# Performance work log

Hardware: AMD Instinct MI355X
Metric: run time of the kernel (lower is better)

Reference implementation:

```python
import jax, jax.numpy as jnp
import numpy as np

B, S, D = 4, 2048, 2048


def setup_inputs() -> dict:
    key = jax.random.key(0)
    ks = jax.random.split(key, 24)
    sc = 1.0 / np.sqrt(D)
    def lin(ki, kb):
        W = jax.random.normal(ks[ki], (D, D), dtype=jnp.float32) * sc
        b = jax.random.normal(ks[kb], (D,), dtype=jnp.float32) * 0.01
        return W, b
    Wi, bWi = lin(0, 1); Ui, bUi = lin(2, 3)
    Wf, bWf = lin(4, 5); Uf, bUf = lin(6, 7)
    Wc, bWc = lin(8, 9); Uc, bUc = lin(10, 11)
    Wo, bWo = lin(12, 13); Uo, bUo = lin(14, 15)
    Wp, bp = lin(16, 17)
    x = jax.random.normal(ks[18], (B, S, D), dtype=jnp.float32)
    h = jax.random.normal(ks[19], (B, S, D), dtype=jnp.float32)
    return dict(x=x, h=h, Wi=Wi, bWi=bWi, Ui=Ui, bUi=bUi,
                Wf=Wf, bWf=bWf, Uf=Uf, bUf=bUf,
                Wc=Wc, bWc=bWc, Uc=Uc, bUc=bUc,
                Wo=Wo, bWo=bWo, Uo=Uo, bUo=bUo,
                Wp=Wp, bp=bp)


def reference(x, h, Wi, bWi, Ui, bUi, Wf, bWf, Uf, bUf,
              Wc, bWc, Uc, bUc, Wo, bWo, Uo, bUo, Wp, bp):
    # In the torch source, h[:, t, :] is read BEFORE being overwritten at step t,
    # and c is zero-initialized with each slot written once (so f * c_prev == 0).
    # Hence the computation is exactly parallel over the time axis.
    Zi = jnp.einsum('bsd,ed->bse', x, Wi) + bWi + jnp.einsum('bsd,ed->bse', h, Ui) + bUi
    Zf = jnp.einsum('bsd,ed->bse', x, Wf) + bWf + jnp.einsum('bsd,ed->bse', h, Uf) + bUf
    Zc = jnp.einsum('bsd,ed->bse', x, Wc) + bWc + jnp.einsum('bsd,ed->bse', h, Uc) + bUc
    Zo = jnp.einsum('bsd,ed->bse', x, Wo) + bWo + jnp.einsum('bsd,ed->bse', h, Uo) + bUo
    i = jnp.exp(Zi)
    f = jnp.exp(Zf)  # multiplies a zero cell state in the source; kept for fidelity
    c = f * jnp.zeros_like(f) + i * jnp.tanh(Zc)
    h_out = jax.nn.sigmoid(Zo) * jnp.tanh(c)
    hidden_state = h_out[:, -1, :] @ Wp.T + bp
    return (hidden_state, c)
```

## Files before the change

### kernel.cpp

```cpp
#include <hip/hip_runtime.h>
#include <hip/hip_bf16.h>

typedef short short8 __attribute__((ext_vector_type(8)));
typedef unsigned short ushort8v __attribute__((ext_vector_type(8)));
typedef float f32x4 __attribute__((ext_vector_type(4)));

#define D_DIM 2048
#define KTOT 4096
#define M_TOT 8192
#define NPACK 4096


__device__ __forceinline__ unsigned short f2bf(float f) {
    union { float f; unsigned u; } c; c.f = f;
    unsigned u = c.u;
    u += 0x7fffu + ((u >> 16) & 1u);
    return (unsigned short)(u >> 16);
}

__device__ __forceinline__ float fast_tanh(float x) {
    float ax = fabsf(x);
    float ez = __expf(2.0f * fminf(ax, 15.0f));
    float t = (ez - 1.0f) / (ez + 1.0f);
    return copysignf(t, x);
}

#define GLOAD_LDS16(g, l)                                                     \
    __builtin_amdgcn_global_load_lds(                                         \
        (const __attribute__((address_space(1))) void*)(g),                   \
        (__attribute__((address_space(3))) void*)(l), 16, 0, 0)

#define WAITVM_(N) asm volatile("s_waitcnt vmcnt(" #N ")" ::: "memory")
#define WAITVM(N)  WAITVM_(N)
#define WAITLG_(N) asm volatile("s_waitcnt lgkmcnt(" #N ")" ::: "memory")
#define WAITLG(N)  WAITLG_(N)
#define BAR        __builtin_amdgcn_s_barrier()
#define SCHB       __builtin_amdgcn_sched_barrier(0)
#define PRIO1      __builtin_amdgcn_s_setprio(1)
#define PRIO0      __builtin_amdgcn_s_setprio(0)


__global__ __launch_bounds__(256)
void pack2(const float* __restrict__ X, const float* __restrict__ H,
           __hip_bfloat16* __restrict__ dst, int total8) {
    int t = blockIdx.x * 256 + threadIdx.x;
    if (t >= total8) return;
    long e0 = (long)t * 8;
    long r  = e0 >> 12;
    int  k  = (int)(e0 & 4095);
    const float* src = (k < D_DIM) ? (X + r * D_DIM + k)
                                   : (H + r * D_DIM + (k - D_DIM));
    float4 v0 = *(const float4*)(src);
    float4 v1 = *(const float4*)(src + 4);
    ushort8v o;
    o[0] = f2bf(v0.x); o[1] = f2bf(v0.y); o[2] = f2bf(v0.z); o[3] = f2bf(v0.w);
    o[4] = f2bf(v1.x); o[5] = f2bf(v1.y); o[6] = f2bf(v1.z); o[7] = f2bf(v1.w);
    *(ushort8v*)(dst + e0) = o;
}


__global__ __launch_bounds__(256)
void pack_gates(const float* __restrict__ Wi, const float* __restrict__ Ui,
                const float* __restrict__ Wc, const float* __restrict__ Uc,
                __hip_bfloat16* __restrict__ dst) {
    int t = blockIdx.x * 256 + threadIdx.x;
    const int g = t >> 9;
    const int k = (t & 511) * 8;
    const int w = g & 31;
    const int n = ((g >> 5) << 4) | (w & 15);
    const float* Wm = (w & 16) ? Wc : Wi;
    const float* Um = (w & 16) ? Uc : Ui;
    const float* src = (k < D_DIM) ? (Wm + (size_t)n * D_DIM + k)
                                   : (Um + (size_t)n * D_DIM + (k - D_DIM));
    float4 v0 = *(const float4*)(src);
    float4 v1 = *(const float4*)(src + 4);
    ushort8v o;
    o[0] = f2bf(v0.x); o[1] = f2bf(v0.y); o[2] = f2bf(v0.z); o[3] = f2bf(v0.w);
    o[4] = f2bf(v1.x); o[5] = f2bf(v1.y); o[6] = f2bf(v1.z); o[7] = f2bf(v1.w);
    *(ushort8v*)(dst + (size_t)g * KTOT + k) = o;
}


__device__ __forceinline__ f32x4 mf(short8 a, short8 b, f32x4 c) {
    return __builtin_amdgcn_mfma_f32_16x16x32_bf16(a, b, c, 0, 0, 0);
}

#define RD4A(BUF, IMM)                                                        \
  { _Pragma("unroll") for (int m_ = 0; m_ < 4; ++m_) {                        \
      ak0[m_] = *(const short8*)(rdA0 + (BUF) + (IMM) + m_ * 2048);           \
      ak1[m_] = *(const short8*)(rdA1 + (BUF) + (IMM) + m_ * 2048); } }

#define RDB(d0, d1, BUF, IMM)                                                 \
  { _Pragma("unroll") for (int n_ = 0; n_ < 2; ++n_) {                        \
      d0[n_] = *(const short8*)(rdB0 + (BUF) + (IMM) + n_ * 2048);            \
      d1[n_] = *(const short8*)(rdB1 + (BUF) + (IMM) + n_ * 2048); } }

#define MF16(MB, NB, bk0, bk1)                                                \
  { _Pragma("unroll") for (int m_ = 0; m_ < 4; ++m_)                          \
    _Pragma("unroll") for (int n_ = 0; n_ < 2; ++n_)                          \
      acc[(MB)+m_][(NB)+n_] = mf(ak0[m_], bk0[n_], acc[(MB)+m_][(NB)+n_]);    \
    _Pragma("unroll") for (int m_ = 0; m_ < 4; ++m_)                          \
    _Pragma("unroll") for (int n_ = 0; n_ < 2; ++n_)                          \
      acc[(MB)+m_][(NB)+n_] = mf(ak1[m_], bk1[n_], acc[(MB)+m_][(NB)+n_]); }

#define SA0(BUFB, KB) { GLOAD_LDS16(gAh0 + (KB), ldsA + (BUFB) + dOff);       \
                        GLOAD_LDS16(gAh0 + (KB) + 524288, ldsA + (BUFB) + dOff + 8192); }
#define SA1(BUFB, KB) { GLOAD_LDS16(gAh1 + (KB), ldsA + (BUFB) + 16384 + dOff); \
                        GLOAD_LDS16(gAh1 + (KB) + 524288, ldsA + (BUFB) + 16384 + dOff + 8192); }
#define SB0(BUFB, KB) { GLOAD_LDS16(gBh0 + (KB), ldsB + (BUFB) + dOff);       \
                        GLOAD_LDS16(gBh0 + (KB) + 524288, ldsB + (BUFB) + dOff + 8192); }
#define SB1(BUFB, KB) { GLOAD_LDS16(gBh1 + (KB), ldsB + (BUFB) + 16384 + dOff); \
                        GLOAD_LDS16(gBh1 + (KB) + 524288, ldsB + (BUFB) + 16384 + dOff + 8192); }

#define KTILE(BUF, S1, S2, S3, S4, VMN)                                       \
  {            \
    RD4A(BUF, 0);                                                             \
    RDB(b01k0, b01k1, BUF, 0);                                                \
    S1;                                                                       \
    WAITLG(8);                                                                \
    BAR; WAITLG(0); SCHB;                                                     \
    PRIO1; MF16(0, 0, b01k0, b01k1); PRIO0; BAR;                              \
                                 \
    RDB(b23k0, b23k1, BUF, 4096);                                             \
    S2;                                                                       \
    BAR; WAITLG(0); SCHB;                                                     \
    PRIO1; MF16(0, 2, b23k0, b23k1); PRIO0; BAR;                              \
                                 \
    RD4A(BUF, 8192);                                                          \
    S3;                                                                       \
    BAR; WAITLG(0); SCHB;                                                     \
    PRIO1; MF16(4, 0, b01k0, b01k1); PRIO0; BAR;                              \
                          \
    S4; VMN;                                                                  \
    BAR; SCHB;                                                                \
    PRIO1; MF16(4, 2, b23k0, b23k1); PRIO0; BAR;                              \
  }

#define NOSTG (void)0

__global__ __launch_bounds__(512, 2)
void gemm8(const __hip_bfloat16* __restrict__ A,
           const __hip_bfloat16* __restrict__ Bp,
           const float* __restrict__ bWi, const float* __restrict__ bUi,
           const float* __restrict__ bWc, const float* __restrict__ bUc,
           float* __restrict__ Cout) {
    __shared__ __hip_bfloat16 sA[2][2][128][64];
    __shared__ __hip_bfloat16 sB[2][2][128][64];

    const int tid  = threadIdx.x;
    const int wid  = tid >> 6;
    const int lane = tid & 63;

    int bid = blockIdx.x;
    bid = (bid & 7) * 64 + (bid >> 3);
    const int tn = (bid & 15) * 256;
    const int tm = (bid >> 4) * 256;

    const int wr  = (wid >> 2) * 128;
    const int wc  = (wid & 3) * 64;
    const int r15 = lane & 15;
    const int g   = lane >> 4;

    const int sb    = g ^ (r15 & 3);
    const int khb   = (r15 >> 2) & 1;
    const int slot0 = (khb * 4 + sb) * 16;
    const int slot1 = (((1 ^ khb) * 4) + sb) * 16;

    const char* rdA0 = (const char*)sA + (wr >> 7) * 16384 + r15 * 128 + slot0;
    const char* rdA1 = (const char*)sA + (wr >> 7) * 16384 + r15 * 128 + slot1;
    const char* rdB0 = (const char*)sB + (wc >> 7) * 16384 + (wc & 64) * 128 + r15 * 128 + slot0;
    const char* rdB1 = (const char*)sB + (wc >> 7) * 16384 + (wc & 64) * 128 + r15 * 128 + slot1;

    const int r0 = tid >> 3, s0 = tid & 7;
    const int colb = (((s0 >> 2) ^ ((r0 >> 2) & 1)) * 64) +
                     (((s0 & 3) ^ (r0 & 3)) * 16);
    const char* gAh0 = (const char*)(A  + (size_t)(tm + r0) * KTOT) + colb;
    const char* gAh1 = gAh0 + (size_t)128 * KTOT * 2;
    const char* gBh0 = (const char*)(Bp + (size_t)(tn + r0) * KTOT) + colb;
    const char* gBh1 = gBh0 + (size_t)128 * KTOT * 2;
    char* ldsA = (char*)sA;
    char* ldsB = (char*)sB;
    const int dOff = tid * 16;

    f32x4 acc[8][4] = {};
    short8 ak0[4], ak1[4], b01k0[2], b01k1[2], b23k0[2], b23k1[2];

    SB0(0, 0); SB1(0, 0); SA0(0, 0); SA1(0, 0);
    SB0(32768, 128); SB1(32768, 128);
    WAITVM(4);
    BAR;

    int kb = 0;
    #pragma unroll 1
    for (int i = 0; i < 31; ++i) {
        KTILE(0,
              SA0(32768, kb + 128), SA1(32768, kb + 128),
              SB0(0, kb + 256),     SB1(0, kb + 256),
              WAITVM(4));
        KTILE(32768,
              SA0(0, kb + 256),     SA1(0, kb + 256),
              SB0(32768, kb + 384), SB1(32768, kb + 384),
              WAITVM(4));
        kb += 256;
    }
    KTILE(0, SA0(32768, kb + 128), SA1(32768, kb + 128),
          NOSTG, NOSTG, WAITVM(0));
    KTILE(32768, NOSTG, NOSTG, NOSTG, NOSTG, NOSTG);

    const int rg4 = (lane >> 4) * 4;
    #pragma unroll
    for (int q = 0; q < 2; ++q) {
        const int gn = (tn >> 1) + (wc >> 1) + q * 16 + r15;
        const float bi_ = bWi[gn] + bUi[gn];
        const float bc_ = bWc[gn] + bUc[gn];
        #pragma unroll
        for (int m = 0; m < 8; ++m) {
            const int gm = tm + wr + m * 16 + rg4;
            #pragma unroll
            for (int r = 0; r < 4; ++r) {
                const float zi = acc[m][2 * q][r]     + bi_;
                const float zc = acc[m][2 * q + 1][r] + bc_;
                Cout[(size_t)(gm + r) * D_DIM + gn] = __expf(zi) * fast_tanh(zc);
            }
        }
    }
}


__global__ __launch_bounds__(256)
void last_gate(const float* __restrict__ x, const float* __restrict__ h,
               const float* __restrict__ Wo, const float* __restrict__ bWo,
               const float* __restrict__ Uo, const float* __restrict__ bUo,
               const float* __restrict__ cfull, float* __restrict__ hbuf) {
    const int o    = blockIdx.x * 4 + (threadIdx.x >> 6);
    const int lane = threadIdx.x & 63;
    const int b = o >> 11, e = o & 2047;
    const float* xr = x  + ((size_t)b * D_DIM + (D_DIM - 1)) * D_DIM;
    const float* hr = h  + ((size_t)b * D_DIM + (D_DIM - 1)) * D_DIM;
    const float* wo = Wo + (size_t)e * D_DIM;
    const float* uo = Uo + (size_t)e * D_DIM;
    float s = 0.0f;
    for (int d = lane; d < D_DIM; d += 64)
        s += xr[d] * wo[d] + hr[d] * uo[d];
    #pragma unroll
    for (int off = 32; off; off >>= 1) s += __shfl_down(s, off);
    if (lane == 0) {
        const float zo  = s + bWo[e] + bUo[e];
        const float sig = 1.0f / (1.0f + __expf(-zo));
        const float cv  = cfull[((size_t)b * D_DIM + (D_DIM - 1)) * D_DIM + e];
        hbuf[o] = sig * fast_tanh(cv);
    }
}


__global__ __launch_bounds__(256)
void proj(const float* __restrict__ hbuf, const float* __restrict__ Wp,
          const float* __restrict__ bp, float* __restrict__ out) {
    const int o    = blockIdx.x * 4 + (threadIdx.x >> 6);
    const int lane = threadIdx.x & 63;
    const int b = o >> 11, p = o & 2047;
    const float* hv = hbuf + (size_t)b * D_DIM;
    const float* wp = Wp   + (size_t)p * D_DIM;
    float s = 0.0f;
    for (int e = lane; e < D_DIM; e += 64)
        s += hv[e] * wp[e];
    #pragma unroll
    for (int off = 32; off; off >>= 1) s += __shfl_down(s, off);
    if (lane == 0) out[o] = s + bp[p];
}


extern "C" void kernel_launch(void* const* d_in, const int* in_sizes, int n_in,
                              void* d_out, int out_size, void* d_ws, size_t ws_size,
                              hipStream_t stream) {
    const float* x   = (const float*)d_in[0];
    const float* h   = (const float*)d_in[1];
    const float* Wi  = (const float*)d_in[2];  const float* bWi = (const float*)d_in[3];
    const float* Ui  = (const float*)d_in[4];  const float* bUi = (const float*)d_in[5];
    const float* Wc  = (const float*)d_in[10]; const float* bWc = (const float*)d_in[11];
    const float* Uc  = (const float*)d_in[12]; const float* bUc = (const float*)d_in[13];
    const float* Wo  = (const float*)d_in[14]; const float* bWo = (const float*)d_in[15];
    const float* Uo  = (const float*)d_in[16]; const float* bUo = (const float*)d_in[17];
    const float* Wp  = (const float*)d_in[18]; const float* bp  = (const float*)d_in[19];

    float* out = (float*)d_out;
    char*  ws  = (char*)d_ws;

    __hip_bfloat16* Abf  = (__hip_bfloat16*)ws;
    __hip_bfloat16* Bpk  = (__hip_bfloat16*)(ws + ((size_t)64 << 20));
    float*          hbuf = (float*)(ws + ((size_t)96 << 20));

    pack2<<<16384, 256, 0, stream>>>(x, h, Abf, M_TOT * KTOT / 8);
    pack_gates<<<8192, 256, 0, stream>>>(Wi, Ui, Wc, Uc, Bpk);

    gemm8<<<(M_TOT / 256) * (NPACK / 256), 512, 0, stream>>>(
        Abf, Bpk, bWi, bUi, bWc, bUc, out + 8192);

    last_gate<<<2048, 256, 0, stream>>>(x, h, Wo, bWo, Uo, bUo, out + 8192,
                                        (float*)hbuf);
    proj<<<2048, 256, 0, stream>>>(hbuf, Wp, bp, out);
}
```

Measured before the change: 320.3 us.

## Triple-buffer A tiles in LDS and deepen prefetch pipeline for GEMM

Allocates a third LDS buffer for the A operand, so A is prefetched two k-tiles ahead while B stays double-buffered. The main loop becomes a six-tile rotation and all global-to-LDS loads are moved into the later stages of each k-tile. Launch bounds drop from 2 to 1 blocks per CU to fit the extra LDS. The intent is to hide more global-load latency, at the cost of occupancy and a more complex wait-count schedule.

```diff
diff --git a/kernel.cpp b/kernel.cpp
--- a/kernel.cpp
+++ b/kernel.cpp
@@ -85,15 +85,15 @@
     return __builtin_amdgcn_mfma_f32_16x16x32_bf16(a, b, c, 0, 0, 0);
 }
 
-#define RD4A(BUF, IMM)                                                        \
+#define RD4A(RGO, IMM)                                                        \
   { _Pragma("unroll") for (int m_ = 0; m_ < 4; ++m_) {                        \
-      ak0[m_] = *(const short8*)(rdA0 + (BUF) + (IMM) + m_ * 2048);           \
-      ak1[m_] = *(const short8*)(rdA1 + (BUF) + (IMM) + m_ * 2048); } }
-
-#define RDB(d0, d1, BUF, IMM)                                                 \
+      ak0[m_] = *(const short8*)(rdA0 + (RGO) + (IMM) + m_ * 2048);           \
+      ak1[m_] = *(const short8*)(rdA1 + (RGO) + (IMM) + m_ * 2048); } }
+
+#define RDB(d0, d1, BFO, IMM)                                                 \
   { _Pragma("unroll") for (int n_ = 0; n_ < 2; ++n_) {                        \
-      d0[n_] = *(const short8*)(rdB0 + (BUF) + (IMM) + n_ * 2048);            \
-      d1[n_] = *(const short8*)(rdB1 + (BUF) + (IMM) + n_ * 2048); } }
+      d0[n_] = *(const short8*)(rdB0 + (BFO) + (IMM) + n_ * 2048);            \
+      d1[n_] = *(const short8*)(rdB1 + (BFO) + (IMM) + n_ * 2048); } }
 
 #define MF16(MB, NB, bk0, bk1)                                                \
   { _Pragma("unroll") for (int m_ = 0; m_ < 4; ++m_)                          \
@@ -103,48 +103,47 @@
     _Pragma("unroll") for (int n_ = 0; n_ < 2; ++n_)                          \
       acc[(MB)+m_][(NB)+n_] = mf(ak1[m_], bk1[n_], acc[(MB)+m_][(NB)+n_]); }
 
-#define SA0(BUFB, KB) { GLOAD_LDS16(gAh0 + (KB), ldsA + (BUFB) + dOff);       \
-                        GLOAD_LDS16(gAh0 + (KB) + 524288, ldsA + (BUFB) + dOff + 8192); }
-#define SA1(BUFB, KB) { GLOAD_LDS16(gAh1 + (KB), ldsA + (BUFB) + 16384 + dOff); \
-                        GLOAD_LDS16(gAh1 + (KB) + 524288, ldsA + (BUFB) + 16384 + dOff + 8192); }
-#define SB0(BUFB, KB) { GLOAD_LDS16(gBh0 + (KB), ldsB + (BUFB) + dOff);       \
-                        GLOAD_LDS16(gBh0 + (KB) + 524288, ldsB + (BUFB) + dOff + 8192); }
-#define SB1(BUFB, KB) { GLOAD_LDS16(gBh1 + (KB), ldsB + (BUFB) + 16384 + dOff); \
-                        GLOAD_LDS16(gBh1 + (KB) + 524288, ldsB + (BUFB) + 16384 + dOff + 8192); }
-
-#define KTILE(BUF, S1, S2, S3, S4, VMN)                                       \
+#define SA0(RGO, KB) { GLOAD_LDS16(gAh0 + (KB), ldsA + (RGO) + dOff);         \
+                       GLOAD_LDS16(gAh0 + (KB) + 524288, ldsA + (RGO) + dOff + 8192); }
+#define SA1(RGO, KB) { GLOAD_LDS16(gAh1 + (KB), ldsA + (RGO) + 16384 + dOff); \
+                       GLOAD_LDS16(gAh1 + (KB) + 524288, ldsA + (RGO) + 16384 + dOff + 8192); }
+#define SB0(BFO, KB) { GLOAD_LDS16(gBh0 + (KB), ldsB + (BFO) + dOff);         \
+                       GLOAD_LDS16(gBh0 + (KB) + 524288, ldsB + (BFO) + dOff + 8192); }
+#define SB1(BFO, KB) { GLOAD_LDS16(gBh1 + (KB), ldsB + (BFO) + 16384 + dOff); \
+                       GLOAD_LDS16(gBh1 + (KB) + 524288, ldsB + (BFO) + 16384 + dOff + 8192); }
+
+#define KTILE(RGO, BFO, S3, S4, VMN)                                          \
   {            \
-    RD4A(BUF, 0);                                                             \
-    RDB(b01k0, b01k1, BUF, 0);                                                \
-    S1;                                                                       \
+    RD4A(RGO, 0);                                                             \
+    RDB(b01k0, b01k1, BFO, 0);                                                \
     WAITLG(8);                                                                \
     BAR; WAITLG(0); SCHB;                                                     \
     PRIO1; MF16(0, 0, b01k0, b01k1); PRIO0; BAR;                              \
                                  \
-    RDB(b23k0, b23k1, BUF, 4096);                                             \
-    S2;                                                                       \
+    RDB(b23k0, b23k1, BFO, 4096);                                             \
     BAR; WAITLG(0); SCHB;                                                     \
     PRIO1; MF16(0, 2, b23k0, b23k1); PRIO0; BAR;                              \
-                                 \
-    RD4A(BUF, 8192);                                                          \
+                \
+    RD4A(RGO, 8192);                                                          \
     S3;                                                                       \
     BAR; WAITLG(0); SCHB;                                                     \
     PRIO1; MF16(4, 0, b01k0, b01k1); PRIO0; BAR;                              \
-                          \
+                  \
     S4; VMN;                                                                  \
     BAR; SCHB;                                                                \
     PRIO1; MF16(4, 2, b23k0, b23k1); PRIO0; BAR;                              \
   }
 
 #define NOSTG (void)0
-
-__global__ __launch_bounds__(512, 2)
+#define NOVM  (void)0
+
+__global__ __launch_bounds__(512, 1)
 void gemm8(const __hip_bfloat16* __restrict__ A,
            const __hip_bfloat16* __restrict__ Bp,
            const float* __restrict__ bWi, const float* __restrict__ bUi,
            const float* __restrict__ bWc, const float* __restrict__ bUc,
            float* __restrict__ Cout) {
-    __shared__ __hip_bfloat16 sA[2][2][128][64];
+    __shared__ __hip_bfloat16 sA[3][2][128][64];
     __shared__ __hip_bfloat16 sB[2][2][128][64];
 
     const int tid  = threadIdx.x;
@@ -185,27 +184,53 @@
     f32x4 acc[8][4] = {};
     short8 ak0[4], ak1[4], b01k0[2], b01k1[2], b23k0[2], b23k1[2];
 
-    SB0(0, 0); SB1(0, 0); SA0(0, 0); SA1(0, 0);
-    SB0(32768, 128); SB1(32768, 128);
-    WAITVM(4);
+    SA0(0, 0);          SA1(0, 0);
+    SB0(0, 0);          SB1(0, 0);
+    SA0(32768, 128);    SA1(32768, 128);
+    SB0(32768, 128);    SB1(32768, 128);
+    SA0(65536, 256);    SA1(65536, 256);
+    WAITVM(12);
     BAR;
 
     int kb = 0;
     #pragma unroll 1
-    for (int i = 0; i < 31; ++i) {
-        KTILE(0,
-              SA0(32768, kb + 128), SA1(32768, kb + 128),
-              SB0(0, kb + 256),     SB1(0, kb + 256),
-              WAITVM(4));
-        KTILE(32768,
-              SA0(0, kb + 256),     SA1(0, kb + 256),
-              SB0(32768, kb + 384), SB1(32768, kb + 384),
-              WAITVM(4));
-        kb += 256;
+    for (int i = 0; i < 10; ++i) {
+        KTILE(0,     0,
+              SB0(0, kb + 256),
+              { SB1(0, kb + 256); SA0(0, kb + 384); SA1(0, kb + 384); },
+              WAITVM(12));
+        KTILE(32768, 32768,
+              SB0(32768, kb + 384),
+              { SB1(32768, kb + 384); SA0(32768, kb + 512); SA1(32768, kb + 512); },
+              WAITVM(12));
+        KTILE(65536, 0,
+              SB0(0, kb + 512),
+              { SB1(0, kb + 512); SA0(65536, kb + 640); SA1(65536, kb + 640); },
+              WAITVM(12));
+        KTILE(0,     32768,
+              SB0(32768, kb + 640),
+              { SB1(32768, kb + 640); SA0(0, kb + 768); SA1(0, kb + 768); },
+              WAITVM(12));
+        KTILE(32768, 0,
+              SB0(0, kb + 768),
+              { SB1(0, kb + 768); SA0(32768, kb + 896); SA1(32768, kb + 896); },
+              WAITVM(12));
+        KTILE(65536, 32768,
+              SB0(32768, kb + 896),
+              { SB1(32768, kb + 896); SA0(65536, kb + 1024); SA1(65536, kb + 1024); },
+              WAITVM(12));
+        kb += 768;
     }
-    KTILE(0, SA0(32768, kb + 128), SA1(32768, kb + 128),
-          NOSTG, NOSTG, WAITVM(0));
-    KTILE(32768, NOSTG, NOSTG, NOSTG, NOSTG, NOSTG);
+    KTILE(0,     0,
+          SB0(0, 7680 + 256),
+          { SB1(0, 7680 + 256); SA0(0, 7680 + 384); SA1(0, 7680 + 384); },
+          WAITVM(12));
+    KTILE(32768, 32768,
+          SB0(32768, 7680 + 384),
+          { SB1(32768, 7680 + 384); },
+          WAITVM(8));
+    KTILE(65536, 0, NOSTG, NOSTG, WAITVM(0));
+    KTILE(0,     32768, NOSTG, NOSTG, NOVM);
 
     const int rg4 = (lane >> 4) * 4;
     #pragma unroll
```

After: 323.0 us. No clear change (+0.9%).

## Restructure GEMM k-tile pipeline into two MFMA phases with merged staging

Applied to the files above, without the earlier changes.

Each k-tile now runs in two phases of 32 MFMAs instead of four phases of 16, with B fragments for both column halves read up front. All A and all B global-to-LDS staging are grouped into one call each, and the prologue and epilogue are rearranged around the new schedule. The aim is fewer barriers and waits per tile and longer uninterrupted MFMA bursts. In exchange, more fragment registers are live at once, and the changed prefetch distance and wait counts risk exposing memory latency or hurting occupancy.

```diff
diff --git a/kernel.cpp b/kernel.cpp
--- a/kernel.cpp
+++ b/kernel.cpp
@@ -103,40 +103,34 @@
     _Pragma("unroll") for (int n_ = 0; n_ < 2; ++n_)                          \
       acc[(MB)+m_][(NB)+n_] = mf(ak1[m_], bk1[n_], acc[(MB)+m_][(NB)+n_]); }
 
-#define SA0(BUFB, KB) { GLOAD_LDS16(gAh0 + (KB), ldsA + (BUFB) + dOff);       \
-                        GLOAD_LDS16(gAh0 + (KB) + 524288, ldsA + (BUFB) + dOff + 8192); }
-#define SA1(BUFB, KB) { GLOAD_LDS16(gAh1 + (KB), ldsA + (BUFB) + 16384 + dOff); \
-                        GLOAD_LDS16(gAh1 + (KB) + 524288, ldsA + (BUFB) + 16384 + dOff + 8192); }
-#define SB0(BUFB, KB) { GLOAD_LDS16(gBh0 + (KB), ldsB + (BUFB) + dOff);       \
-                        GLOAD_LDS16(gBh0 + (KB) + 524288, ldsB + (BUFB) + dOff + 8192); }
-#define SB1(BUFB, KB) { GLOAD_LDS16(gBh1 + (KB), ldsB + (BUFB) + 16384 + dOff); \
+#define SA(BUFB, KB) { GLOAD_LDS16(gAh0 + (KB), ldsA + (BUFB) + dOff);        \
+                       GLOAD_LDS16(gAh0 + (KB) + 524288, ldsA + (BUFB) + dOff + 8192); \
+                       GLOAD_LDS16(gAh1 + (KB), ldsA + (BUFB) + 16384 + dOff); \
+                       GLOAD_LDS16(gAh1 + (KB) + 524288, ldsA + (BUFB) + 16384 + dOff + 8192); }
+#define SBt(BUFB, KB) { GLOAD_LDS16(gBh0 + (KB), ldsB + (BUFB) + dOff);       \
+                        GLOAD_LDS16(gBh0 + (KB) + 524288, ldsB + (BUFB) + dOff + 8192); \
+                        GLOAD_LDS16(gBh1 + (KB), ldsB + (BUFB) + 16384 + dOff); \
                         GLOAD_LDS16(gBh1 + (KB) + 524288, ldsB + (BUFB) + 16384 + dOff + 8192); }
 
-#define KTILE(BUF, S1, S2, S3, S4, VMN)                                       \
-  {            \
+#define KTILE(BUF, S_A, S_B, VMN)                                             \
+  {                                                                  \
     RD4A(BUF, 0);                                                             \
     RDB(b01k0, b01k1, BUF, 0);                                                \
-    S1;                                                                       \
+    RDB(b23k0, b23k1, BUF, 4096);                                             \
+    S_A;                                                                      \
     WAITLG(8);                                                                \
     BAR; WAITLG(0); SCHB;                                                     \
-    PRIO1; MF16(0, 0, b01k0, b01k1); PRIO0; BAR;                              \
-                                 \
-    RDB(b23k0, b23k1, BUF, 4096);                                             \
-    S2;                                                                       \
+    PRIO1; MF16(0, 0, b01k0, b01k1); MF16(0, 2, b23k0, b23k1); PRIO0; BAR;    \
+                                                                     \
+    RD4A(BUF, 8192);                                                          \
+    S_B;                                                                      \
+    VMN;                                                                      \
     BAR; WAITLG(0); SCHB;                                                     \
-    PRIO1; MF16(0, 2, b23k0, b23k1); PRIO0; BAR;                              \
-                                 \
-    RD4A(BUF, 8192);                                                          \
-    S3;                                                                       \
-    BAR; WAITLG(0); SCHB;                                                     \
-    PRIO1; MF16(4, 0, b01k0, b01k1); PRIO0; BAR;                              \
-                          \
-    S4; VMN;                                                                  \
-    BAR; SCHB;                                                                \
-    PRIO1; MF16(4, 2, b23k0, b23k1); PRIO0; BAR;                              \
+    PRIO1; MF16(4, 0, b01k0, b01k1); MF16(4, 2, b23k0, b23k1); PRIO0; BAR;    \
   }
 
 #define NOSTG (void)0
+#define NOVM  (void)0
 
 __global__ __launch_bounds__(512, 2)
 void gemm8(const __hip_bfloat16* __restrict__ A,
@@ -185,27 +179,23 @@
     f32x4 acc[8][4] = {};
     short8 ak0[4], ak1[4], b01k0[2], b01k1[2], b23k0[2], b23k1[2];
 
-    SB0(0, 0); SB1(0, 0); SA0(0, 0); SA1(0, 0);
-    SB0(32768, 128); SB1(32768, 128);
-    WAITVM(4);
+    SA(0, 0);          SBt(0, 0);
+    SA(32768, 128);    SBt(32768, 128);
+    WAITVM(8);
     BAR;
+
+    KTILE(0, NOSTG, SBt(0, 256), WAITVM(4));
 
     int kb = 0;
     #pragma unroll 1
-    for (int i = 0; i < 31; ++i) {
-        KTILE(0,
-              SA0(32768, kb + 128), SA1(32768, kb + 128),
-              SB0(0, kb + 256),     SB1(0, kb + 256),
-              WAITVM(4));
-        KTILE(32768,
-              SA0(0, kb + 256),     SA1(0, kb + 256),
-              SB0(32768, kb + 384), SB1(32768, kb + 384),
-              WAITVM(4));
+    for (int i = 0; i < 30; ++i) {
+        KTILE(32768, SA(0, kb + 256),     SBt(32768, kb + 384), WAITVM(4));
+        KTILE(0,     SA(32768, kb + 384), SBt(0, kb + 512),     WAITVM(4));
         kb += 256;
     }
-    KTILE(0, SA0(32768, kb + 128), SA1(32768, kb + 128),
-          NOSTG, NOSTG, WAITVM(0));
-    KTILE(32768, NOSTG, NOSTG, NOSTG, NOSTG, NOSTG);
+    KTILE(32768, SA(0, 7936), SBt(32768, 8064), WAITVM(4));
+    KTILE(0,     SA(32768, 8064), NOSTG,        WAITVM(0));
+    KTILE(32768, NOSTG, NOSTG, NOVM);
 
     const int rg4 = (lane >> 4) * 4;
     #pragma unroll
```

Measured after the change: 318.2 us. No clear change (-0.6%).
